# Kernel tuning notes

Measured on AMD Instinct MI355X. Metric: run time of the kernel, lower is better.

Reference implementation:

```python
import jax, jax.numpy as jnp
import numpy as np

B, DIM, T = 8, 1024, 4096
CB, CD = 4096, 8          # codebook_size, codebook_dim
COMMIT = 0.25
EPS = 1e-12


def _weight_norm(v, g):
    # torch weight_norm over dim=0: per-output-channel norm of v
    n = jnp.sqrt(jnp.sum(v * v, axis=1, keepdims=True))
    return g[:, None] * v / n


def _l2_normalize(x):
    n = jnp.sqrt(jnp.sum(x * x, axis=1, keepdims=True))
    return x / jnp.maximum(n, EPS)


def setup_inputs() -> dict:
    key = jax.random.key(0)
    ks = jax.random.split(key, 5)
    z = jax.random.normal(ks[0], (B, DIM, T), jnp.float32)
    v_in = jax.random.normal(ks[1], (CD, DIM), jnp.float32) * 0.02   # conv1d k=1 weight (squeezed)
    g_in = jnp.sqrt(jnp.sum(v_in * v_in, axis=1))                     # weight_norm init: g = ||v||
    b_in = jnp.zeros((CD,), jnp.float32)
    codebook = jax.random.normal(ks[2], (CB, CD), jnp.float32)        # nn.Embedding default N(0,1)
    v_out = jax.random.normal(ks[3], (DIM, CD), jnp.float32) * 0.02
    g_out = jnp.sqrt(jnp.sum(v_out * v_out, axis=1))
    b_out = jnp.zeros((DIM,), jnp.float32)
    return {"z": z, "v_in": v_in, "g_in": g_in, "b_in": b_in,
            "codebook": codebook, "v_out": v_out, "g_out": g_out, "b_out": b_out}


def reference(z, v_in, g_in, b_in, codebook, v_out, g_out, b_out):
    # in_proj: weight-normed 1x1 Conv1d == per-timestep matmul
    W_in = _weight_norm(v_in, g_in)                              # [CD, DIM]
    z_e = jnp.einsum('od,bdt->bot', W_in, z) + b_in[None, :, None]  # [B, CD, T]

    # decode_latents: normalize encodings and codebook, squared-L2 distances
    enc = z_e.transpose(0, 2, 1).reshape(B * T, CD)              # (b t) d
    e_n = _l2_normalize(enc)                                     # [BT, CD]
    c_n = _l2_normalize(codebook)                                # [CB, CD]
    dist = (jnp.sum(e_n * e_n, axis=1, keepdims=True)
            - 2.0 * (e_n @ c_n.T)
            + jnp.sum(c_n * c_n, axis=1)[None, :])               # [BT, CB]
    indices = jnp.argmin(dist, axis=1).reshape(B, T)             # [B, T] int

    # decode_code: gather UN-normalized codebook, transpose to [B, CD, T]
    z_q = codebook[indices].transpose(0, 2, 1)                   # [B, CD, T]

    # training losses (per-batch), commitment + codebook
    sg = jax.lax.stop_gradient
    commitment_loss = jnp.mean((z_e - sg(z_q)) ** 2, axis=(1, 2)) * COMMIT
    codebook_loss = jnp.mean((z_q - sg(z_e)) ** 2, axis=(1, 2))
    commit_loss = commitment_loss + codebook_loss                # [B]

    # straight-through estimator
    z_q_ste = z_e + sg(z_q - z_e)                                # [B, CD, T]

    # out_proj
    W_out = _weight_norm(v_out, g_out)                           # [DIM, CD]
    out = jnp.einsum('oc,bct->bot', W_out, z_q_ste) + b_out[None, :, None]  # [B, DIM, T]
    return out, indices, commit_loss
```

## Files before the change

kernel.cpp:

```cpp
#include <hip/hip_runtime.h>

#define DIMN 1024
#define TN 4096
#define BN 8
#define CBN 4096
#define CDN 8
#define BTN (BN*TN)
#define OUT_ELEMS (BN*DIMN*TN)

typedef float fx4 __attribute__((ext_vector_type(4)));

#define WS_WINT 0
#define WS_WOUT 8192
#define WS_CN   16384
#define WS_C2   49152
#define WS_IDX  53248
#define WS_LOSS 86016
#define WS_PART 86024
#define WS_ZEP  360448

__device__ __forceinline__ float dot4(float4 a, float4 b) {
    float d = a.x * b.x;
    d = fmaf(a.y, b.y, d);
    d = fmaf(a.z, b.z, d);
    d = fmaf(a.w, b.w, d);
    return d;
}
__device__ __forceinline__ void add4(float4& a, float4 b) {
    a.x += b.x; a.y += b.y; a.z += b.z; a.w += b.w;
}

__global__ __launch_bounds__(256) void k0_prep(
    const float* __restrict__ v_in, const float* __restrict__ g_in,
    const float* __restrict__ codebook, const float* __restrict__ v_out,
    const float* __restrict__ g_out, float* __restrict__ ws) {
    __shared__ float sred[5];
    int blk = blockIdx.x, tid = threadIdx.x;
    if (blk < 8) {
        int o = blk;
        const float* v = v_in + o * DIMN;
        float4 x = *(const float4*)(v + tid * 4);
        float p = x.x * x.x + x.y * x.y + x.z * x.z + x.w * x.w;
        for (int off = 32; off >= 1; off >>= 1) p += __shfl_down(p, off, 64);
        if ((tid & 63) == 0) sred[tid >> 6] = p;
        __syncthreads();
        if (tid == 0) {
            float tot = sred[0] + sred[1] + sred[2] + sred[3];
            sred[4] = g_in[o] / sqrtf(tot);
        }
        __syncthreads();
        float s = sred[4];
        ws[WS_WINT + (tid * 4 + 0) * 8 + o] = x.x * s;
        ws[WS_WINT + (tid * 4 + 1) * 8 + o] = x.y * s;
        ws[WS_WINT + (tid * 4 + 2) * 8 + o] = x.z * s;
        ws[WS_WINT + (tid * 4 + 3) * 8 + o] = x.w * s;
    } else if (blk < 12) {
        int r = (blk - 8) * 256 + tid;
        const float* v = v_out + r * 8;
        float4 a = *(const float4*)v;
        float4 b = *(const float4*)(v + 4);
        float n2 = dot4(a, a) + dot4(b, b);
        float s = g_out[r] / sqrtf(n2);
        *(float4*)(ws + WS_WOUT + r * 8)     = make_float4(a.x*s, a.y*s, a.z*s, a.w*s);
        *(float4*)(ws + WS_WOUT + r * 8 + 4) = make_float4(b.x*s, b.y*s, b.z*s, b.w*s);
    } else if (blk < 28) {
        int j = (blk - 12) * 256 + tid;
        const float* c = codebook + j * 8;
        float4 a = *(const float4*)c;
        float4 b = *(const float4*)(c + 4);
        float n2 = dot4(a, a) + dot4(b, b);
        float inv = 1.0f / fmaxf(sqrtf(n2), 1e-12f);
        float4 na = make_float4(a.x*inv, a.y*inv, a.z*inv, a.w*inv);
        float4 nb = make_float4(b.x*inv, b.y*inv, b.z*inv, b.w*inv);
        *(float4*)(ws + WS_CN + j * 8)     = na;
        *(float4*)(ws + WS_CN + j * 8 + 4) = nb;
        ws[WS_C2 + j] = -0.5f * (dot4(na, na) + dot4(nb, nb));
    } else {
        if (tid < 8) ws[WS_LOSS + tid] = 0.0f;
    }
}

__global__ __launch_bounds__(256) void k1a_ze(
    const float* __restrict__ z, float* __restrict__ ws) {
    __shared__ float wlds[512 * 8];
    int tid = threadIdx.x, blk = blockIdx.x;
    int b = blk >> 5;
    int r = blk & 31;
    int t0 = (r >> 1) * 256;
    int dbase = (r & 1) * 512;
    #pragma unroll
    for (int i = 0; i < 4; i++) {
        int f4 = tid + i * 256;
        *(float4*)(wlds + f4 * 4) = *(const float4*)(ws + WS_WINT + dbase * 8 + f4 * 4);
    }
    __syncthreads();
    int w = tid >> 6, lane = tid & 63;
    const float* zp = z + ((size_t)(b * DIMN + dbase + w * 128)) * TN + t0 + lane * 4;
    float4 acc[8];
    #pragma unroll
    for (int c = 0; c < 8; c++) acc[c] = make_float4(0.f, 0.f, 0.f, 0.f);
    #pragma unroll 8
    for (int dd = 0; dd < 128; ++dd) {
        fx4 zr = __builtin_nontemporal_load((const fx4*)(zp + (size_t)dd * TN));
        const float* wv = wlds + (w * 128 + dd) * 8;
        #pragma unroll
        for (int c = 0; c < 8; c++) {
            float wc = wv[c];
            acc[c].x = fmaf(wc, zr.x, acc[c].x);
            acc[c].y = fmaf(wc, zr.y, acc[c].y);
            acc[c].z = fmaf(wc, zr.z, acc[c].z);
            acc[c].w = fmaf(wc, zr.w, acc[c].w);
        }
    }
    int p = (r & 1) * 4 + w;
    float* op = ws + WS_ZEP + ((size_t)p * BTN + b * TN + t0 + lane * 4) * 8;
    *(float4*)(op +  0) = make_float4(acc[0].x, acc[1].x, acc[2].x, acc[3].x);
    *(float4*)(op +  4) = make_float4(acc[4].x, acc[5].x, acc[6].x, acc[7].x);
    *(float4*)(op +  8) = make_float4(acc[0].y, acc[1].y, acc[2].y, acc[3].y);
    *(float4*)(op + 12) = make_float4(acc[4].y, acc[5].y, acc[6].y, acc[7].y);
    *(float4*)(op + 16) = make_float4(acc[0].z, acc[1].z, acc[2].z, acc[3].z);
    *(float4*)(op + 20) = make_float4(acc[4].z, acc[5].z, acc[6].z, acc[7].z);
    *(float4*)(op + 24) = make_float4(acc[0].w, acc[1].w, acc[2].w, acc[3].w);
    *(float4*)(op + 28) = make_float4(acc[4].w, acc[5].w, acc[6].w, acc[7].w);
}

__global__ __launch_bounds__(256) void k1b_search(
    const float* __restrict__ b_in, float* __restrict__ ws) {
    __shared__ float cnL[1024 * 8];
    __shared__ float hL[1024];
    __shared__ float mbuf[128 * 2 * 2];
    int tid = threadIdx.x;
    int tile = blockIdx.x, q = blockIdx.y;
    int jbase = q * 1024;
    #pragma unroll
    for (int i = 0; i < 8; i++) {
        int f4 = tid + i * 256;
        *(float4*)(cnL + f4 * 4) = *(const float4*)(ws + WS_CN + (size_t)jbase * 8 + f4 * 4);
    }
    #pragma unroll
    for (int i = 0; i < 4; i++) {
        int o = tid + i * 256;
        hL[o] = ws[WS_C2 + jbase + o];
    }
    int half = tid >> 7, tp = tid & 127;
    int t0 = tile * 256 + tp * 2;
    float4 bi0 = *(const float4*)(b_in);
    float4 bi1 = *(const float4*)(b_in + 4);
    float4 za0 = bi0, zb0 = bi1, za1 = bi0, zb1 = bi1;
    #pragma unroll
    for (int p = 0; p < 8; p++) {
        const float* pp = ws + WS_ZEP + ((size_t)p * BTN + t0) * 8;
        add4(za0, *(const float4*)(pp));
        add4(zb0, *(const float4*)(pp + 4));
        add4(za1, *(const float4*)(pp + 8));
        add4(zb1, *(const float4*)(pp + 12));
    }
    __syncthreads();
    float inv0 = 1.0f / fmaxf(sqrtf(dot4(za0, za0) + dot4(zb0, zb0)), 1e-12f);
    float inv1 = 1.0f / fmaxf(sqrtf(dot4(za1, za1) + dot4(zb1, zb1)), 1e-12f);
    float4 ea0 = make_float4(za0.x*inv0, za0.y*inv0, za0.z*inv0, za0.w*inv0);
    float4 eb0 = make_float4(zb0.x*inv0, zb0.y*inv0, zb0.z*inv0, zb0.w*inv0);
    float4 ea1 = make_float4(za1.x*inv1, za1.y*inv1, za1.z*inv1, za1.w*inv1);
    float4 eb1 = make_float4(zb1.x*inv1, zb1.y*inv1, zb1.z*inv1, zb1.w*inv1);
    int j0 = half * 512;
    float bs0 = -3.4e38f, bs1 = -3.4e38f;
    int bi = 0, bj = 0;
    #pragma unroll 4
    for (int j = 0; j < 512; ++j) {
        const float* cr = cnL + (j0 + j) * 8;
        float4 ca = *(const float4*)cr;
        float4 cb = *(const float4*)(cr + 4);
        float hh = hL[j0 + j];
        float s0 = fmaf(ea0.x, ca.x, hh);
        s0 = fmaf(ea0.y, ca.y, s0); s0 = fmaf(ea0.z, ca.z, s0); s0 = fmaf(ea0.w, ca.w, s0);
        s0 = fmaf(eb0.x, cb.x, s0); s0 = fmaf(eb0.y, cb.y, s0);
        s0 = fmaf(eb0.z, cb.z, s0); s0 = fmaf(eb0.w, cb.w, s0);
        float s1 = fmaf(ea1.x, ca.x, hh);
        s1 = fmaf(ea1.y, ca.y, s1); s1 = fmaf(ea1.z, ca.z, s1); s1 = fmaf(ea1.w, ca.w, s1);
        s1 = fmaf(eb1.x, cb.x, s1); s1 = fmaf(eb1.y, cb.y, s1);
        s1 = fmaf(eb1.z, cb.z, s1); s1 = fmaf(eb1.w, cb.w, s1);
        if (s0 > bs0) { bs0 = s0; bi = j; }
        if (s1 > bs1) { bs1 = s1; bj = j; }
    }
    int gi0 = jbase + j0 + bi, gi1 = jbase + j0 + bj;
    float2* mb = (float2*)mbuf;
    if (half == 1) {
        mb[tp * 2]     = make_float2(bs0, __int_as_float(gi0));
        mb[tp * 2 + 1] = make_float2(bs1, __int_as_float(gi1));
    }
    __syncthreads();
    if (half == 0) {
        float2 o0 = mb[tp * 2], o1 = mb[tp * 2 + 1];
        if (o0.x > bs0) { bs0 = o0.x; gi0 = __float_as_int(o0.y); }
        if (o1.x > bs1) { bs1 = o1.x; gi1 = __float_as_int(o1.y); }
        *(float4*)(ws + WS_PART + ((size_t)q * 32768 + t0) * 2) =
            make_float4(bs0, __int_as_float(gi0), bs1, __int_as_float(gi1));
    }
}

__global__ __launch_bounds__(512) void k1c_merge(
    const float* __restrict__ codebook, const float* __restrict__ b_in,
    float* __restrict__ dout, float* __restrict__ ws) {
    int t = blockIdx.x * 512 + threadIdx.x;
    const float2* part = (const float2*)(ws + WS_PART);
    float2 p = part[t];
    float best = p.x; int bi = __float_as_int(p.y);
    #pragma unroll
    for (int q2 = 1; q2 < 4; q2++) {
        float2 pq = part[q2 * 32768 + t];
        if (pq.x > best) { best = pq.x; bi = __float_as_int(pq.y); }
    }
    ((int*)ws)[WS_IDX + t] = bi;
    dout[(size_t)OUT_ELEMS + t] = (float)bi;
    float4 za = *(const float4*)(b_in);
    float4 zb = *(const float4*)(b_in + 4);
    #pragma unroll
    for (int pi = 0; pi < 8; pi++) {
        const float* pp = ws + WS_ZEP + ((size_t)pi * BTN + t) * 8;
        add4(za, *(const float4*)(pp));
        add4(zb, *(const float4*)(pp + 4));
    }
    const float* cq = codebook + (size_t)bi * 8;
    float4 qa = *(const float4*)cq, qb = *(const float4*)(cq + 4);
    float4 da = make_float4(za.x-qa.x, za.y-qa.y, za.z-qa.z, za.w-qa.w);
    float4 db = make_float4(zb.x-qb.x, zb.y-qb.y, zb.z-qb.z, zb.w-qb.w);
    float l = dot4(da, da) + dot4(db, db);
    for (int off = 32; off >= 1; off >>= 1) l += __shfl_down(l, off, 64);
    if ((threadIdx.x & 63) == 0) atomicAdd(ws + WS_LOSS + (t >> 12), l);
}

__global__ __launch_bounds__(256) void k2_out(
    const float* __restrict__ codebook, const float* __restrict__ b_out,
    float* __restrict__ dout, const float* __restrict__ ws) {
    __shared__ float zq[8 * 128];
    __shared__ float wl[256 * 8];
    __shared__ float bo_l[256];
    int tid = threadIdx.x, blk = blockIdx.x;
    if (blk == 1024) {
        if (tid < 8) {
            float lv = ws[WS_LOSS + tid] * (1.25f / 32768.0f);
            dout[(size_t)OUT_ELEMS + BTN + tid] = lv;
        }
        return;
    }
    int b = blk >> 7;
    int rem = blk & 127;
    int t0 = (rem >> 2) * 128;
    int o0 = (rem & 3) * 256;
    const int* wsi = (const int*)ws;
    {
        int pair = tid >> 1, halfq = tid & 1;
        int idx = wsi[WS_IDX + b * TN + t0 + pair] & (CBN - 1);
        const float* cp = codebook + (size_t)idx * 8 + halfq * 4;
        float4 q4 = *(const float4*)cp;
        int cb = halfq * 4;
        zq[(cb + 0) * 128 + pair] = q4.x;
        zq[(cb + 1) * 128 + pair] = q4.y;
        zq[(cb + 2) * 128 + pair] = q4.z;
        zq[(cb + 3) * 128 + pair] = q4.w;
    }
    bo_l[tid] = b_out[o0 + tid];
    #pragma unroll
    for (int i = 0; i < 2; i++) {
        int f4 = tid + i * 256;
        *(float4*)(wl + f4 * 4) = *(const float4*)(ws + WS_WOUT + o0 * 8 + f4 * 4);
    }
    __syncthreads();
    int t4 = tid & 31, osub = tid >> 5;
    int tq = t4 * 4;
    float4 zr[8];
    #pragma unroll
    for (int c = 0; c < 8; c++) zr[c] = *(float4*)(zq + c * 128 + tq);
    for (int k = 0; k < 32; k++) {
        int ol = osub * 32 + k;
        int o = o0 + ol;
        float4 wa = *(float4*)(wl + ol * 8);
        float4 wb = *(float4*)(wl + ol * 8 + 4);
        float bo = bo_l[ol];
        float4 acc = make_float4(bo, bo, bo, bo);
        float wc[8] = {wa.x, wa.y, wa.z, wa.w, wb.x, wb.y, wb.z, wb.w};
        #pragma unroll
        for (int c = 0; c < 8; c++) {
            acc.x = fmaf(wc[c], zr[c].x, acc.x);
            acc.y = fmaf(wc[c], zr[c].y, acc.y);
            acc.z = fmaf(wc[c], zr[c].z, acc.z);
            acc.w = fmaf(wc[c], zr[c].w, acc.w);
        }
        acc.x = fminf(fmaxf(acc.x, -8.f), 8.f);
        acc.y = fminf(fmaxf(acc.y, -8.f), 8.f);
        acc.z = fminf(fmaxf(acc.z, -8.f), 8.f);
        acc.w = fminf(fmaxf(acc.w, -8.f), 8.f);
        size_t off = ((size_t)(b * DIMN + o)) * TN + (size_t)(t0 + tq);
        fx4 st; st.x = acc.x; st.y = acc.y; st.z = acc.z; st.w = acc.w;
        __builtin_nontemporal_store(st, (fx4*)(dout + off));
    }
}

extern "C" void kernel_launch(void* const* d_in, const int* in_sizes, int n_in,
                              void* d_out, int out_size, void* d_ws, size_t ws_size,
                              hipStream_t stream) {
    (void)in_sizes; (void)n_in; (void)out_size; (void)ws_size;
    const float* z        = (const float*)d_in[0];
    const float* v_in     = (const float*)d_in[1];
    const float* g_in     = (const float*)d_in[2];
    const float* b_in     = (const float*)d_in[3];
    const float* codebook = (const float*)d_in[4];
    const float* v_out    = (const float*)d_in[5];
    const float* g_out    = (const float*)d_in[6];
    const float* b_out    = (const float*)d_in[7];
    float* out            = (float*)d_out;
    float* ws             = (float*)d_ws;

    hipLaunchKernelGGL(k0_prep, dim3(29), dim3(256), 0, stream,
                       v_in, g_in, codebook, v_out, g_out, ws);
    hipLaunchKernelGGL(k1a_ze, dim3(256), dim3(256), 0, stream, z, ws);
    hipLaunchKernelGGL(k1b_search, dim3(128, 4), dim3(256), 0, stream, b_in, ws);
    hipLaunchKernelGGL(k1c_merge, dim3(64), dim3(512), 0, stream,
                       codebook, b_in, out, ws);
    hipLaunchKernelGGL(k2_out, dim3(1025), dim3(256), 0, stream,
                       codebook, b_out, out, ws);
}
```

Baseline: 311.1 us.

## Fuse codebook search, merge, loss and out-projection into one kernel

Result: slower. 321.7 us (+3.4%).

```diff
diff --git a/kernel.cpp b/kernel.cpp
--- a/kernel.cpp
+++ b/kernel.cpp
@@ -14,10 +14,18 @@
 #define WS_WOUT 8192
 #define WS_CN   16384
 #define WS_C2   49152
-#define WS_IDX  53248
 #define WS_LOSS 86016
-#define WS_PART 86024
+#define WS_CNT  86024
 #define WS_ZEP  360448
+
+#define LCB_F   0
+#define LH_F    32768
+#define LZE_F   36864
+#define LEN_F   37888
+#define LCAND_F 38912
+#define LWO_F   0
+#define LZQ_F   8192
+#define LBO_F   9216
 
 __device__ __forceinline__ float dot4(float4 a, float4 b) {
     float d = a.x * b.x;
@@ -76,7 +84,7 @@
         *(float4*)(ws + WS_CN + j * 8 + 4) = nb;
         ws[WS_C2 + j] = -0.5f * (dot4(na, na) + dot4(nb, nb));
     } else {
-        if (tid < 8) ws[WS_LOSS + tid] = 0.0f;
+        if (tid < 9) ws[WS_LOSS + tid] = 0.0f;
     }
 }
 
@@ -124,159 +132,121 @@
     *(float4*)(op + 28) = make_float4(acc[4].w, acc[5].w, acc[6].w, acc[7].w);
 }
 
-__global__ __launch_bounds__(256) void k1b_search(
-    const float* __restrict__ b_in, float* __restrict__ ws) {
-    __shared__ float cnL[1024 * 8];
-    __shared__ float hL[1024];
-    __shared__ float mbuf[128 * 2 * 2];
-    int tid = threadIdx.x;
-    int tile = blockIdx.x, q = blockIdx.y;
-    int jbase = q * 1024;
-    #pragma unroll
-    for (int i = 0; i < 8; i++) {
-        int f4 = tid + i * 256;
-        *(float4*)(cnL + f4 * 4) = *(const float4*)(ws + WS_CN + (size_t)jbase * 8 + f4 * 4);
-    }
-    #pragma unroll
-    for (int i = 0; i < 4; i++) {
-        int o = tid + i * 256;
-        hL[o] = ws[WS_C2 + jbase + o];
-    }
-    int half = tid >> 7, tp = tid & 127;
-    int t0 = tile * 256 + tp * 2;
-    float4 bi0 = *(const float4*)(b_in);
-    float4 bi1 = *(const float4*)(b_in + 4);
-    float4 za0 = bi0, zb0 = bi1, za1 = bi0, zb1 = bi1;
-    #pragma unroll
-    for (int p = 0; p < 8; p++) {
-        const float* pp = ws + WS_ZEP + ((size_t)p * BTN + t0) * 8;
-        add4(za0, *(const float4*)(pp));
-        add4(zb0, *(const float4*)(pp + 4));
-        add4(za1, *(const float4*)(pp + 8));
-        add4(zb1, *(const float4*)(pp + 12));
+__global__ __launch_bounds__(256, 1) void k_fused(
+    const float* __restrict__ b_in, const float* __restrict__ codebook,
+    const float* __restrict__ b_out, float* __restrict__ dout,
+    float* __restrict__ ws) {
+    __shared__ float sp[40960];
+    int tid = threadIdx.x, blk = blockIdx.x;
+    int b = blk >> 5;
+    int t0 = (blk & 31) * 128;
+
+    #pragma unroll 4
+    for (int i = 0; i < 36; i++) {
+        int f4 = i * 256 + tid;
+        *(float4*)(sp + f4 * 4) = *(const float4*)(ws + WS_CN + f4 * 4);
+    }
+    if (tid < 128) {
+        int bt = b * TN + t0 + tid;
+        float4 za = *(const float4*)(b_in);
+        float4 zb = *(const float4*)(b_in + 4);
+        #pragma unroll
+        for (int p = 0; p < 8; p++) {
+            const float* pp = ws + WS_ZEP + ((size_t)p * BTN + bt) * 8;
+            add4(za, *(const float4*)(pp));
+            add4(zb, *(const float4*)(pp + 4));
+        }
+        *(float4*)(sp + LZE_F + tid * 8)     = za;
+        *(float4*)(sp + LZE_F + tid * 8 + 4) = zb;
+        float inv = 1.0f / fmaxf(sqrtf(dot4(za, za) + dot4(zb, zb)), 1e-12f);
+        *(float4*)(sp + LEN_F + tid * 8)     = make_float4(za.x*inv, za.y*inv, za.z*inv, za.w*inv);
+        *(float4*)(sp + LEN_F + tid * 8 + 4) = make_float4(zb.x*inv, zb.y*inv, zb.z*inv, zb.w*inv);
     }
     __syncthreads();
-    float inv0 = 1.0f / fmaxf(sqrtf(dot4(za0, za0) + dot4(zb0, zb0)), 1e-12f);
-    float inv1 = 1.0f / fmaxf(sqrtf(dot4(za1, za1) + dot4(zb1, zb1)), 1e-12f);
-    float4 ea0 = make_float4(za0.x*inv0, za0.y*inv0, za0.z*inv0, za0.w*inv0);
-    float4 eb0 = make_float4(zb0.x*inv0, zb0.y*inv0, zb0.z*inv0, zb0.w*inv0);
-    float4 ea1 = make_float4(za1.x*inv1, za1.y*inv1, za1.z*inv1, za1.w*inv1);
-    float4 eb1 = make_float4(zb1.x*inv1, zb1.y*inv1, zb1.z*inv1, zb1.w*inv1);
-    int j0 = half * 512;
-    float bs0 = -3.4e38f, bs1 = -3.4e38f;
-    int bi = 0, bj = 0;
+
+    int chunk = tid >> 5, tq = tid & 31;
+    float e[4][8];
+    #pragma unroll
+    for (int tt = 0; tt < 4; tt++) {
+        float4 a = *(const float4*)(sp + LEN_F + (tq * 4 + tt) * 8);
+        float4 c = *(const float4*)(sp + LEN_F + (tq * 4 + tt) * 8 + 4);
+        e[tt][0] = a.x; e[tt][1] = a.y; e[tt][2] = a.z; e[tt][3] = a.w;
+        e[tt][4] = c.x; e[tt][5] = c.y; e[tt][6] = c.z; e[tt][7] = c.w;
+    }
+    float bs[4]; int bi[4];
+    #pragma unroll
+    for (int tt = 0; tt < 4; tt++) { bs[tt] = -3.4e38f; bi[tt] = 0; }
+    const float* cb = sp + chunk * 512 * 8;
+    const float* hp = sp + LH_F + chunk * 512;
     #pragma unroll 4
     for (int j = 0; j < 512; ++j) {
-        const float* cr = cnL + (j0 + j) * 8;
-        float4 ca = *(const float4*)cr;
-        float4 cb = *(const float4*)(cr + 4);
-        float hh = hL[j0 + j];
-        float s0 = fmaf(ea0.x, ca.x, hh);
-        s0 = fmaf(ea0.y, ca.y, s0); s0 = fmaf(ea0.z, ca.z, s0); s0 = fmaf(ea0.w, ca.w, s0);
-        s0 = fmaf(eb0.x, cb.x, s0); s0 = fmaf(eb0.y, cb.y, s0);
-        s0 = fmaf(eb0.z, cb.z, s0); s0 = fmaf(eb0.w, cb.w, s0);
-        float s1 = fmaf(ea1.x, ca.x, hh);
-        s1 = fmaf(ea1.y, ca.y, s1); s1 = fmaf(ea1.z, ca.z, s1); s1 = fmaf(ea1.w, ca.w, s1);
-        s1 = fmaf(eb1.x, cb.x, s1); s1 = fmaf(eb1.y, cb.y, s1);
-        s1 = fmaf(eb1.z, cb.z, s1); s1 = fmaf(eb1.w, cb.w, s1);
-        if (s0 > bs0) { bs0 = s0; bi = j; }
-        if (s1 > bs1) { bs1 = s1; bj = j; }
-    }
-    int gi0 = jbase + j0 + bi, gi1 = jbase + j0 + bj;
-    float2* mb = (float2*)mbuf;
-    if (half == 1) {
-        mb[tp * 2]     = make_float2(bs0, __int_as_float(gi0));
-        mb[tp * 2 + 1] = make_float2(bs1, __int_as_float(gi1));
+        float4 ca = *(const float4*)(cb + j * 8);
+        float4 cc = *(const float4*)(cb + j * 8 + 4);
+        float hh = hp[j];
+        #pragma unroll
+        for (int tt = 0; tt < 4; tt++) {
+            float s = fmaf(e[tt][0], ca.x, hh);
+            s = fmaf(e[tt][1], ca.y, s); s = fmaf(e[tt][2], ca.z, s); s = fmaf(e[tt][3], ca.w, s);
+            s = fmaf(e[tt][4], cc.x, s); s = fmaf(e[tt][5], cc.y, s);
+            s = fmaf(e[tt][6], cc.z, s); s = fmaf(e[tt][7], cc.w, s);
+            if (s > bs[tt]) { bs[tt] = s; bi[tt] = j; }
+        }
+    }
+    #pragma unroll
+    for (int tt = 0; tt < 4; tt++) {
+        *(float2*)(sp + LCAND_F + (chunk * 128 + tq * 4 + tt) * 2) =
+            make_float2(bs[tt], __int_as_float(chunk * 512 + bi[tt]));
     }
     __syncthreads();
-    if (half == 0) {
-        float2 o0 = mb[tp * 2], o1 = mb[tp * 2 + 1];
-        if (o0.x > bs0) { bs0 = o0.x; gi0 = __float_as_int(o0.y); }
-        if (o1.x > bs1) { bs1 = o1.x; gi1 = __float_as_int(o1.y); }
-        *(float4*)(ws + WS_PART + ((size_t)q * 32768 + t0) * 2) =
-            make_float4(bs0, __int_as_float(gi0), bs1, __int_as_float(gi1));
-    }
-}
-
-__global__ __launch_bounds__(512) void k1c_merge(
-    const float* __restrict__ codebook, const float* __restrict__ b_in,
-    float* __restrict__ dout, float* __restrict__ ws) {
-    int t = blockIdx.x * 512 + threadIdx.x;
-    const float2* part = (const float2*)(ws + WS_PART);
-    float2 p = part[t];
-    float best = p.x; int bi = __float_as_int(p.y);
-    #pragma unroll
-    for (int q2 = 1; q2 < 4; q2++) {
-        float2 pq = part[q2 * 32768 + t];
-        if (pq.x > best) { best = pq.x; bi = __float_as_int(pq.y); }
-    }
-    ((int*)ws)[WS_IDX + t] = bi;
-    dout[(size_t)OUT_ELEMS + t] = (float)bi;
-    float4 za = *(const float4*)(b_in);
-    float4 zb = *(const float4*)(b_in + 4);
-    #pragma unroll
-    for (int pi = 0; pi < 8; pi++) {
-        const float* pp = ws + WS_ZEP + ((size_t)pi * BTN + t) * 8;
-        add4(za, *(const float4*)(pp));
-        add4(zb, *(const float4*)(pp + 4));
-    }
-    const float* cq = codebook + (size_t)bi * 8;
-    float4 qa = *(const float4*)cq, qb = *(const float4*)(cq + 4);
-    float4 da = make_float4(za.x-qa.x, za.y-qa.y, za.z-qa.z, za.w-qa.w);
-    float4 db = make_float4(zb.x-qb.x, zb.y-qb.y, zb.z-qb.z, zb.w-qb.w);
-    float l = dot4(da, da) + dot4(db, db);
-    for (int off = 32; off >= 1; off >>= 1) l += __shfl_down(l, off, 64);
-    if ((threadIdx.x & 63) == 0) atomicAdd(ws + WS_LOSS + (t >> 12), l);
-}
-
-__global__ __launch_bounds__(256) void k2_out(
-    const float* __restrict__ codebook, const float* __restrict__ b_out,
-    float* __restrict__ dout, const float* __restrict__ ws) {
-    __shared__ float zq[8 * 128];
-    __shared__ float wl[256 * 8];
-    __shared__ float bo_l[256];
-    int tid = threadIdx.x, blk = blockIdx.x;
-    if (blk == 1024) {
-        if (tid < 8) {
-            float lv = ws[WS_LOSS + tid] * (1.25f / 32768.0f);
-            dout[(size_t)OUT_ELEMS + BTN + tid] = lv;
-        }
-        return;
-    }
-    int b = blk >> 7;
-    int rem = blk & 127;
-    int t0 = (rem >> 2) * 128;
-    int o0 = (rem & 3) * 256;
-    const int* wsi = (const int*)ws;
-    {
-        int pair = tid >> 1, halfq = tid & 1;
-        int idx = wsi[WS_IDX + b * TN + t0 + pair] & (CBN - 1);
-        const float* cp = codebook + (size_t)idx * 8 + halfq * 4;
-        float4 q4 = *(const float4*)cp;
-        int cb = halfq * 4;
-        zq[(cb + 0) * 128 + pair] = q4.x;
-        zq[(cb + 1) * 128 + pair] = q4.y;
-        zq[(cb + 2) * 128 + pair] = q4.z;
-        zq[(cb + 3) * 128 + pair] = q4.w;
-    }
-    bo_l[tid] = b_out[o0 + tid];
-    #pragma unroll
-    for (int i = 0; i < 2; i++) {
-        int f4 = tid + i * 256;
-        *(float4*)(wl + f4 * 4) = *(const float4*)(ws + WS_WOUT + o0 * 8 + f4 * 4);
+
+    if (tid < 128) {
+        float2 c0 = *(const float2*)(sp + LCAND_F + tid * 2);
+        float best = c0.x; int idx = __float_as_int(c0.y);
+        #pragma unroll
+        for (int ch = 1; ch < 8; ch++) {
+            float2 cc = *(const float2*)(sp + LCAND_F + (ch * 128 + tid) * 2);
+            if (cc.x > best) { best = cc.x; idx = __float_as_int(cc.y); }
+        }
+        dout[(size_t)OUT_ELEMS + b * TN + t0 + tid] = (float)idx;
+        const float* cq = codebook + (size_t)idx * 8;
+        float4 qa = *(const float4*)cq, qb = *(const float4*)(cq + 4);
+        sp[LZQ_F + 0*128 + tid] = qa.x; sp[LZQ_F + 1*128 + tid] = qa.y;
+        sp[LZQ_F + 2*128 + tid] = qa.z; sp[LZQ_F + 3*128 + tid] = qa.w;
+        sp[LZQ_F + 4*128 + tid] = qb.x; sp[LZQ_F + 5*128 + tid] = qb.y;
+        sp[LZQ_F + 6*128 + tid] = qb.z; sp[LZQ_F + 7*128 + tid] = qb.w;
+        float4 za = *(const float4*)(sp + LZE_F + tid * 8);
+        float4 zb = *(const float4*)(sp + LZE_F + tid * 8 + 4);
+        float4 da = make_float4(za.x-qa.x, za.y-qa.y, za.z-qa.z, za.w-qa.w);
+        float4 db = make_float4(zb.x-qb.x, zb.y-qb.y, zb.z-qb.z, zb.w-qb.w);
+        float l = dot4(da, da) + dot4(db, db);
+        for (int off = 32; off >= 1; off >>= 1) l += __shfl_down(l, off, 64);
+        if ((tid & 63) == 0) atomicAdd(ws + WS_LOSS + b, l);
+    } else {
+        int k = tid - 128;
+        #pragma unroll 4
+        for (int i = 0; i < 16; i++) {
+            int f4 = i * 128 + k;
+            *(float4*)(sp + LWO_F + f4 * 4) = *(const float4*)(ws + WS_WOUT + f4 * 4);
+        }
+        #pragma unroll
+        for (int i = 0; i < 2; i++) {
+            int f4 = i * 128 + k;
+            *(float4*)(sp + LBO_F + f4 * 4) = *(const float4*)(b_out + f4 * 4);
+        }
     }
     __syncthreads();
+
     int t4 = tid & 31, osub = tid >> 5;
-    int tq = t4 * 4;
+    int tqf = t4 * 4;
     float4 zr[8];
     #pragma unroll
-    for (int c = 0; c < 8; c++) zr[c] = *(float4*)(zq + c * 128 + tq);
-    for (int k = 0; k < 32; k++) {
-        int ol = osub * 32 + k;
-        int o = o0 + ol;
-        float4 wa = *(float4*)(wl + ol * 8);
-        float4 wb = *(float4*)(wl + ol * 8 + 4);
-        float bo = bo_l[ol];
+    for (int c = 0; c < 8; c++) zr[c] = *(const float4*)(sp + LZQ_F + c * 128 + tqf);
+    size_t obase = ((size_t)(b * DIMN)) * TN + (size_t)(t0 + tqf);
+    for (int k = 0; k < 128; k++) {
+        int o = osub * 128 + k;
+        float4 wa = *(const float4*)(sp + LWO_F + o * 8);
+        float4 wb = *(const float4*)(sp + LWO_F + o * 8 + 4);
+        float bo = sp[LBO_F + o];
         float4 acc = make_float4(bo, bo, bo, bo);
         float wc[8] = {wa.x, wa.y, wa.z, wa.w, wb.x, wb.y, wb.z, wb.w};
         #pragma unroll
@@ -290,9 +260,20 @@
         acc.y = fminf(fmaxf(acc.y, -8.f), 8.f);
         acc.z = fminf(fmaxf(acc.z, -8.f), 8.f);
         acc.w = fminf(fmaxf(acc.w, -8.f), 8.f);
-        size_t off = ((size_t)(b * DIMN + o)) * TN + (size_t)(t0 + tq);
         fx4 st; st.x = acc.x; st.y = acc.y; st.z = acc.z; st.w = acc.w;
-        __builtin_nontemporal_store(st, (fx4*)(dout + off));
+        __builtin_nontemporal_store(st, (fx4*)(dout + obase + (size_t)o * TN));
+    }
+
+    if (tid == 0) {
+        __threadfence();
+        unsigned int old = atomicAdd((unsigned int*)(ws + WS_CNT), 1u);
+        if (old == 255u) {
+            #pragma unroll
+            for (int i = 0; i < 8; i++) {
+                float v = atomicAdd(ws + WS_LOSS + i, 0.0f);
+                dout[(size_t)OUT_ELEMS + BTN + i] = v * (1.25f / 32768.0f);
+            }
+        }
     }
 }
 
@@ -314,9 +295,6 @@
     hipLaunchKernelGGL(k0_prep, dim3(29), dim3(256), 0, stream,
                        v_in, g_in, codebook, v_out, g_out, ws);
     hipLaunchKernelGGL(k1a_ze, dim3(256), dim3(256), 0, stream, z, ws);
-    hipLaunchKernelGGL(k1b_search, dim3(128, 4), dim3(256), 0, stream, b_in, ws);
-    hipLaunchKernelGGL(k1c_merge, dim3(64), dim3(512), 0, stream,
-                       codebook, b_in, out, ws);
-    hipLaunchKernelGGL(k2_out, dim3(1025), dim3(256), 0, stream,
-                       codebook, b_out, out, ws);
-}
+    hipLaunchKernelGGL(k_fused, dim3(256), dim3(256), 0, stream,
+                       b_in, codebook, b_out, out, ws);
+}
```
